# Kernel optimization log

Measured on AMD Instinct MI355X. Metric: run time of the kernel, lower is better.

Reference implementation:

```python
import jax, jax.numpy as jnp
import numpy as np

B, NP, NC, E, C = 4, 512, 256, 128, 32
NBUCKET = 20


def soft_one_hot_linspace(x, start=0.0, end=15.0, number=NBUCKET):
    # e3nn soft_one_hot_linspace, basis='smooth_finite', cutoff=True
    values = jnp.linspace(start, end, number + 2)[1:-1]
    step = (end - start) / (number + 1)
    diff = (x[..., None] - values) / step

    def sus(y):  # exp(-1/y) for y>0 else 0 (smooth unit step)
        return jnp.where(y > 0.0, jnp.exp(-1.0 / jnp.where(y > 0.0, y, 1.0)), 0.0)

    return 1.14136 * jnp.exp(2.0) * sus(diff + 1.0) * sus(1.0 - diff)


def _init_linear(k, fan_in, fan_out):
    k1, k2 = jax.random.split(k)
    bound = 1.0 / np.sqrt(fan_in)
    W = jax.random.uniform(k1, (fan_in, fan_out), jnp.float32, -bound, bound)
    b = jax.random.uniform(k2, (fan_out,), jnp.float32, -bound, bound)
    return W, b


def setup_inputs() -> dict:
    key = jax.random.key(0)
    ks = jax.random.split(key, 12)
    inp = {}
    inp["z"] = jax.random.normal(ks[0], (B, NP, NC, E), jnp.float32)
    inp["z_mask"] = jax.random.randint(ks[1], (B, NP, NC), 0, 2) == 1
    inp["pocket_rep"] = jax.random.normal(ks[2], (B, NP, E), jnp.float32)
    inp["candidate_dis"] = jax.random.uniform(ks[3], (B, NP, NC), jnp.float32) * 16.0
    inp["W_lin"], inp["b_lin"] = _init_linear(ks[4], E, C)
    inp["W_dis"], inp["b_dis"] = _init_linear(ks[5], NBUCKET, C)
    inp["W_energy"], inp["b_energy"] = _init_linear(ks[6], C, 1)
    inp["W_gate"], inp["b_gate"] = _init_linear(ks[7], C, 1)
    inp["bias"] = jnp.ones((1,), jnp.float32)
    inp["W_energy_p"], inp["b_energy_p"] = _init_linear(ks[8], C, 1)
    inp["W_gate_p"], inp["b_gate_p"] = _init_linear(ks[9], C, 1)
    inp["bias_p"] = jnp.ones((1,), jnp.float32)
    inp["W_out"], inp["b_out"] = _init_linear(ks[10], E * C, E)
    return inp


def reference(z, z_mask, pocket_rep, candidate_dis,
              W_lin, b_lin, W_dis, b_dis,
              W_energy, b_energy, W_gate, b_gate, bias,
              W_energy_p, b_energy_p, W_gate_p, b_gate_p, bias_p,
              W_out, b_out):
    b, n_p, n_c, e = z.shape
    c = W_lin.shape[1]
    # linear + transpose(3,1): [B,Np,Nc,E] -> [B,C,Nc,Np]
    zc = jnp.transpose(z @ W_lin + b_lin, (0, 3, 2, 1))
    # softmax over last dim (Np)
    zc = jax.nn.softmax(zc, axis=-1)
    # distance-bucket bias: [B,Np,Nc,20] -> [B,Np,Nc,C] -> view [B,C,Nc,Np]
    edge_emb = soft_one_hot_linspace(candidate_dis)
    dis_bias = (edge_emb @ W_dis + b_dis).reshape(b, c, n_c, n_p)
    zc = zc + dis_bias
    # z_mask.repeat(C,1,1).view(B,C,Nc,Np) -- literal torch element order
    mask_rep = jnp.tile(z_mask, (c, 1, 1)).reshape(b, c, n_c, n_p)
    zc = jnp.where(mask_rep, jnp.asarray(1e-09, zc.dtype), zc)
    # gated energy heads on z.transpose(3,1): [B,Np,Nc,C]
    zt = jnp.transpose(zc, (0, 3, 2, 1))
    zm = z_mask.astype(zc.dtype)
    pair_energy = (jax.nn.sigmoid(zt @ W_gate + b_gate) * (zt @ W_energy + b_energy))[..., 0] * zm
    affinity_pred = jax.nn.leaky_relu(bias + pair_energy.sum(axis=(-1, -2)))
    pair_energy_p = (jax.nn.sigmoid(zt @ W_gate_p + b_gate_p) * (zt @ W_energy_p + b_energy_p))[..., 0] * zm
    prmsd_pred = jax.nn.leaky_relu(bias_p + pair_energy_p.sum(axis=(-1, -2)))
    # ligand rep: bmm([B,C*Nc,Np], [B,Np,E]) -> [B,Nc,C*E] -> Linear
    lig = jnp.einsum('bcln,bne->bcle', zc, pocket_rep)  # [B,C,Nc,E]
    lig = jnp.transpose(lig, (0, 2, 1, 3)).reshape(b, n_c, c * e)
    ligand_rep = lig @ W_out + b_out
    return (ligand_rep, affinity_pred, prmsd_pred)
```

## Files before the change

### kernel.cpp

```cpp
#include <hip/hip_runtime.h>
#include <stdint.h>


typedef float f32x4 __attribute__((ext_vector_type(4)));
typedef short s16x8 __attribute__((ext_vector_type(8)));

#define DEV static __device__ __forceinline__

DEV unsigned short f2bf(float f) {
  unsigned u = __builtin_bit_cast(unsigned, f);
  u += 0x7FFFu + ((u >> 16) & 1u);
  return (unsigned short)(u >> 16);
}
DEV float bf2f(unsigned short h) {
  unsigned u = ((unsigned)h) << 16;
  return __builtin_bit_cast(float, u);
}

__global__ void prep_k(const float* __restrict__ wlin,
                       const float* __restrict__ pocket,
                       const float* __restrict__ wout,
                       const int* __restrict__ zmask,
                       const float* __restrict__ cdis,
                       const float* __restrict__ bout,
                       unsigned short* __restrict__ wtlin,
                       unsigned short* __restrict__ pt,
                       unsigned short* __restrict__ wto,
                       unsigned long long* __restrict__ zmb,
                       float* __restrict__ cdisT,
                       float* __restrict__ outp,
                       float* __restrict__ accg) {
  for (int i = blockIdx.x * 256 + threadIdx.x; i < 1970184; i += gridDim.x * 256) {
    if (i < 524288) {
      int np = i & 511, nc = (i >> 9) & 255, b = i >> 17;
      unsigned long long bal = __ballot(zmask[b * 131072 + np * 256 + nc] != 0);
      if ((i & 63) == 0) zmb[i >> 6] = bal;
    } else if (i < 1048576) {
      int o = i - 524288;
      int e = o >> 12, k = o & 4095;
      wto[o] = f2bf(wout[k * 128 + e]);
    } else if (i < 1310720) {
      int o = i - 1048576;
      int np = o & 511, r = o >> 9;
      int e = r & 127, b = r >> 7;
      pt[o] = f2bf(pocket[(b * 512 + np) * 128 + e]);
    } else if (i < 1314816) {
      int o = i - 1310720;
      int k = o & 127, c = o >> 7;
      wtlin[o] = f2bf(wlin[k * 32 + c]);
    } else if (i < 1314824) {
      accg[i - 1314816] = 0.0f;
    } else if (i < 1839112) {
      int o = i - 1314824;
      int c = o & 31, np5 = (o >> 5) & 15, nc = (o >> 9) & 255, b = o >> 17;
      cdisT[o] = cdis[(b * 512 + 16 * c + (nc >> 4)) * 256 + 16 * (nc & 15) + np5];
    } else {
      int o = i - 1839112;
      outp[o] = bout[o & 127];
    }
  }
}

extern __shared__ char smem[];

__global__ __launch_bounds__(256, 4) void mega_k(
    const float* __restrict__ z, const int* __restrict__ zmask,
    const float* __restrict__ cdisT,
    const float* __restrict__ wdis, const float* __restrict__ bdis_g,
    const float* __restrict__ wE, const float* __restrict__ bE,
    const float* __restrict__ wG, const float* __restrict__ bG,
    const float* __restrict__ wEp, const float* __restrict__ bEp,
    const float* __restrict__ wGp, const float* __restrict__ bGp,
    const unsigned short* __restrict__ wtlin,
    const unsigned short* __restrict__ pt,
    const unsigned long long* __restrict__ zmb,
    unsigned short* __restrict__ lig, float* __restrict__ accg) {
  const int nc = blockIdx.x, b = blockIdx.y;
  const int t = threadIdx.x;
  const int w = t >> 6, ln = t & 63;
  const int m16 = ln & 15, q = ln >> 4;

  unsigned short* T = (unsigned short*)smem;

  __shared__ float s_wd[640];
  __shared__ float s_bd[32];
  __shared__ float s_we[32], s_wg[32], s_wep[32], s_wgp[32];
  __shared__ float s_red[160];
  __shared__ float s_gmax[32], s_gsum[32];
  __shared__ unsigned long long s_mb[4][8];
  __shared__ float s_r8[8];

  if (t < 32) {
    s_bd[t] = bdis_g[t];
    s_we[t] = wE[t]; s_wg[t] = wG[t];
    s_wep[t] = wEp[t]; s_wgp[t] = wGp[t];
  }
  for (int i = t; i < 640; i += 256) s_wd[i] = wdis[i];
  for (int i = t; i < 2048; i += 256) {
    int cm = i >> 9, nn = i & 511;
    unsigned long long bal = __ballot(zmask[cm * 131072 + nc * 512 + nn] != 0);
    if ((i & 63) == 0) s_mb[cm][nn >> 6] = bal;
  }

  f32x4 acc1[8][2];
#pragma unroll
  for (int i = 0; i < 8; ++i) {
    acc1[i][0] = f32x4{0.f, 0.f, 0.f, 0.f};
    acc1[i][1] = f32x4{0.f, 0.f, 0.f, 0.f};
  }
  const float* zb = z + (size_t)b * 16777216 + (size_t)nc * 128;
  for (int k0 = 0; k0 < 128; k0 += 32) {
    s16x8 bf0 = *(const s16x8*)(wtlin + m16 * 128 + k0 + q * 8);
    s16x8 bf1 = *(const s16x8*)(wtlin + (16 + m16) * 128 + k0 + q * 8);
#pragma unroll
    for (int bt = 0; bt < 4; ++bt) {
      f32x4 z0[2], z1[2];
#pragma unroll
      for (int i = 0; i < 2; ++i) {
        int np = (w * 8 + bt * 2 + i) * 16 + m16;
        const float* p = zb + (size_t)np * 32768 + k0 + q * 8;
        z0[i] = *(const f32x4*)p;
        z1[i] = *(const f32x4*)(p + 4);
      }
#pragma unroll
      for (int i = 0; i < 2; ++i) {
        s16x8 af;
        af[0] = (short)f2bf(z0[i][0]); af[1] = (short)f2bf(z0[i][1]);
        af[2] = (short)f2bf(z0[i][2]); af[3] = (short)f2bf(z0[i][3]);
        af[4] = (short)f2bf(z1[i][0]); af[5] = (short)f2bf(z1[i][1]);
        af[6] = (short)f2bf(z1[i][2]); af[7] = (short)f2bf(z1[i][3]);
        int ai = bt * 2 + i;
        acc1[ai][0] = __builtin_amdgcn_mfma_f32_16x16x32_bf16(af, bf0, acc1[ai][0], 0, 0, 0);
        acc1[ai][1] = __builtin_amdgcn_mfma_f32_16x16x32_bf16(af, bf1, acc1[ai][1], 0, 0, 0);
      }
    }
  }

  float mx[2] = {-3.0e38f, -3.0e38f};
#pragma unroll
  for (int ai = 0; ai < 8; ++ai)
#pragma unroll
    for (int ct = 0; ct < 2; ++ct)
#pragma unroll
      for (int r = 0; r < 4; ++r) mx[ct] = fmaxf(mx[ct], acc1[ai][ct][r]);
#pragma unroll
  for (int ct = 0; ct < 2; ++ct) {
    float v = mx[ct];
    v = fmaxf(v, __shfl_xor(v, 16));
    v = fmaxf(v, __shfl_xor(v, 32));
    mx[ct] = v;
  }
  if (ln < 16) { s_red[ln * 5 + w] = mx[0]; s_red[(16 + ln) * 5 + w] = mx[1]; }
  __syncthreads();
  if (t < 32)
    s_gmax[t] = fmaxf(fmaxf(s_red[t * 5], s_red[t * 5 + 1]),
                      fmaxf(s_red[t * 5 + 2], s_red[t * 5 + 3]));
  __syncthreads();
  float sm[2] = {0.f, 0.f};
#pragma unroll
  for (int ct = 0; ct < 2; ++ct) {
    float g = s_gmax[ct * 16 + m16];
#pragma unroll
    for (int ai = 0; ai < 8; ++ai)
#pragma unroll
      for (int r = 0; r < 4; ++r) {
        float e = __expf(acc1[ai][ct][r] - g);
        acc1[ai][ct][r] = e;
        sm[ct] += e;
      }
  }
#pragma unroll
  for (int ct = 0; ct < 2; ++ct) {
    float v = sm[ct];
    v += __shfl_xor(v, 16);
    v += __shfl_xor(v, 32);
    sm[ct] = v;
  }
  if (ln < 16) { s_red[ln * 5 + w] = sm[0]; s_red[(16 + ln) * 5 + w] = sm[1]; }
  __syncthreads();
  if (t < 32)
    s_gsum[t] = 1.0f / (s_red[t * 5] + s_red[t * 5 + 1] + s_red[t * 5 + 2] + s_red[t * 5 + 3]);
  __syncthreads();

#pragma unroll
  for (int ct = 0; ct < 2; ++ct) {
    int c = ct * 16 + m16;
    float s = s_gsum[c];
#pragma unroll
    for (int ai = 0; ai < 8; ++ai) {
      int npb = (w * 8 + ai) * 16 + q * 4;
      unsigned lo = (unsigned)f2bf(acc1[ai][ct][0] * s) |
                    ((unsigned)f2bf(acc1[ai][ct][1] * s) << 16);
      unsigned hi = (unsigned)f2bf(acc1[ai][ct][2] * s) |
                    ((unsigned)f2bf(acc1[ai][ct][3] * s) << 16);
      *(uint2*)(T + c * 520 + npb) = make_uint2(lo, hi);
    }
  }
  __syncthreads();

  {
    const float SUSK = 8.4335794f;
    const float* cdb = cdisT + (size_t)(b * 256 + nc) * 512;
#pragma unroll
    for (int tt = 0; tt < 2; ++tt) {
      int task = t + tt * 256;
      int c = task & 31, np5 = task >> 5;
      float d = cdb[task];
      float val[32];
#pragma unroll
      for (int kk = 0; kk < 32; ++kk) val[kk] = s_bd[kk];
      for (int j = 0; j < 20; ++j) {
        float diff = d * (21.0f / 15.0f) - (float)(j + 1);
        float y1 = diff + 1.f, y2 = 1.f - diff;
        float u = 0.f;
        if (y1 > 0.f && y2 > 0.f) u = SUSK * __expf(-1.f / y1 - 1.f / y2);
#pragma unroll
        for (int kk = 0; kk < 32; ++kk) val[kk] += u * s_wd[j * 32 + kk];
      }
      int npb = np5 * 32;
      unsigned long long mw = s_mb[c & 3][npb >> 6];
#pragma unroll
      for (int kb2 = 0; kb2 < 4; ++kb2) {
        unsigned short* tp = T + c * 520 + npb + kb2 * 8;
        s16x8 tv = *(s16x8*)tp;
        s16x8 ov;
#pragma unroll
        for (int kk = 0; kk < 8; ++kk) {
          float x = bf2f((unsigned short)tv[kk]) + val[kb2 * 8 + kk];
          int mk = (int)((mw >> ((npb + kb2 * 8 + kk) & 63)) & 1ull);
          ov[kk] = (short)f2bf(mk ? 1e-9f : x);
        }
        *(s16x8*)tp = ov;
      }
    }
  }
  __syncthreads();

  {
    float aff = 0.f, prm = 0.f;
    const float bg0 = bG[0], be0 = bE[0], bgp0 = bGp[0], bep0 = bEp[0];
    const unsigned long long* zw = zmb + (size_t)(b * 256 + nc) * 8;
#pragma unroll
    for (int s = 0; s < 2; ++s) {
      int np = s * 256 + t;
      float g = bg0, e = be0, gp = bgp0, ep = bep0;
      for (int c = 0; c < 32; ++c) {
        float tv = bf2f(T[c * 520 + np]);
        g += tv * s_wg[c]; e += tv * s_we[c];
        gp += tv * s_wgp[c]; ep += tv * s_wep[c];
      }
      if ((zw[np >> 6] >> (np & 63)) & 1ull) {
        aff += e / (1.f + __expf(-g));
        prm += ep / (1.f + __expf(-gp));
      }
    }
#pragma unroll
    for (int d = 32; d >= 1; d >>= 1) {
      aff += __shfl_xor(aff, d);
      prm += __shfl_xor(prm, d);
    }
    if (ln == 0) { s_r8[w] = aff; s_r8[4 + w] = prm; }
    __syncthreads();
    if (t == 0) {
      atomicAdd(accg + b, s_r8[0] + s_r8[1] + s_r8[2] + s_r8[3]);
      atomicAdd(accg + 4 + b, s_r8[4] + s_r8[5] + s_r8[6] + s_r8[7]);
    }
  }

  {
    f32x4 a5[2][2];
    a5[0][0] = f32x4{0.f, 0.f, 0.f, 0.f}; a5[0][1] = a5[0][0];
    a5[1][0] = a5[0][0]; a5[1][1] = a5[0][0];
    const unsigned short* ptb = pt + b * 65536;
    for (int k0 = 0; k0 < 512; k0 += 32) {
      s16x8 aT0 = *(const s16x8*)(T + m16 * 520 + k0 + q * 8);
      s16x8 aT1 = *(const s16x8*)(T + (16 + m16) * 520 + k0 + q * 8);
      s16x8 bP0 = *(const s16x8*)(ptb + (w * 32 + m16) * 512 + k0 + q * 8);
      s16x8 bP1 = *(const s16x8*)(ptb + (w * 32 + 16 + m16) * 512 + k0 + q * 8);
      a5[0][0] = __builtin_amdgcn_mfma_f32_16x16x32_bf16(aT0, bP0, a5[0][0], 0, 0, 0);
      a5[0][1] = __builtin_amdgcn_mfma_f32_16x16x32_bf16(aT0, bP1, a5[0][1], 0, 0, 0);
      a5[1][0] = __builtin_amdgcn_mfma_f32_16x16x32_bf16(aT1, bP0, a5[1][0], 0, 0, 0);
      a5[1][1] = __builtin_amdgcn_mfma_f32_16x16x32_bf16(aT1, bP1, a5[1][1], 0, 0, 0);
    }
    unsigned short* lg = lig + (size_t)(b * 256 + nc) * 4096;
#pragma unroll
    for (int mt = 0; mt < 2; ++mt)
#pragma unroll
      for (int u = 0; u < 2; ++u)
#pragma unroll
        for (int r = 0; r < 4; ++r) {
          int c = mt * 16 + q * 4 + r;
          int e = w * 32 + u * 16 + m16;
          lg[c * 128 + e] = f2bf(a5[mt][u][r]);
        }
  }
}

__global__ __launch_bounds__(256, 2) void proj_k(
    const unsigned short* __restrict__ lig, const unsigned short* __restrict__ wto,
    const float* __restrict__ accg, const float* __restrict__ bias,
    const float* __restrict__ biasp, float* __restrict__ outp) {
  const int mb = blockIdx.x, ks = blockIdx.y;
  const int t = threadIdx.x, w = t >> 6, ln = t & 63;
  const int m16 = ln & 15, q = ln >> 4;
  f32x4 acc[2][8];
#pragma unroll
  for (int mt = 0; mt < 2; ++mt)
#pragma unroll
    for (int nt = 0; nt < 8; ++nt) acc[mt][nt] = f32x4{0.f, 0.f, 0.f, 0.f};
  const int kb = ks * 256;
  for (int k0 = 0; k0 < 256; k0 += 32) {
    s16x8 af[2], bf[8];
#pragma unroll
    for (int mt = 0; mt < 2; ++mt)
      af[mt] = *(const s16x8*)(lig + (size_t)(mb * 128 + (w * 2 + mt) * 16 + m16) * 4096 + kb + k0 + q * 8);
#pragma unroll
    for (int nt = 0; nt < 8; ++nt)
      bf[nt] = *(const s16x8*)(wto + (size_t)(nt * 16 + m16) * 4096 + kb + k0 + q * 8);
#pragma unroll
    for (int mt = 0; mt < 2; ++mt)
#pragma unroll
      for (int nt = 0; nt < 8; ++nt)
        acc[mt][nt] = __builtin_amdgcn_mfma_f32_16x16x32_bf16(af[mt], bf[nt], acc[mt][nt], 0, 0, 0);
  }
#pragma unroll
  for (int mt = 0; mt < 2; ++mt)
#pragma unroll
    for (int nt = 0; nt < 8; ++nt)
#pragma unroll
      for (int r = 0; r < 4; ++r)
        atomicAdd(outp + (size_t)(mb * 128 + (w * 2 + mt) * 16 + q * 4 + r) * 128 + nt * 16 + m16,
                  acc[mt][nt][r]);
  if (mb == 0 && ks == 0 && t < 8) {
    float base = (t < 4) ? bias[0] : biasp[0];
    float x = base + accg[t];
    outp[131072 + t] = (x >= 0.f) ? x : 0.01f * x;
  }
}

extern "C" void kernel_launch(void* const* d_in, const int* in_sizes, int n_in,
                              void* d_out, int out_size, void* d_ws, size_t ws_size,
                              hipStream_t stream) {
  const float* z      = (const float*)d_in[0];
  const int*   zmask  = (const int*)d_in[1];
  const float* pocket = (const float*)d_in[2];
  const float* cdis   = (const float*)d_in[3];
  const float* wlin   = (const float*)d_in[4];
  const float* wdis   = (const float*)d_in[6];
  const float* bdis   = (const float*)d_in[7];
  const float* wE     = (const float*)d_in[8];
  const float* bE     = (const float*)d_in[9];
  const float* wG     = (const float*)d_in[10];
  const float* bG     = (const float*)d_in[11];
  const float* bias   = (const float*)d_in[12];
  const float* wEp    = (const float*)d_in[13];
  const float* bEp    = (const float*)d_in[14];
  const float* wGp    = (const float*)d_in[15];
  const float* bGp    = (const float*)d_in[16];
  const float* biasp  = (const float*)d_in[17];
  const float* wout   = (const float*)d_in[18];
  const float* bout   = (const float*)d_in[19];

  char* ws = (char*)d_ws;
  float* accg                  = (float*)(ws + 0);
  unsigned short* wtlin        = (unsigned short*)(ws + 1024);
  unsigned long long* zmb      = (unsigned long long*)(ws + 16384);
  unsigned short* pt           = (unsigned short*)(ws + 131072);
  float* cdisT                 = (float*)(ws + 655360);
  unsigned short* wto          = (unsigned short*)(ws + 2752512);
  unsigned short* lig          = (unsigned short*)(ws + 4194304);
  float* outp = (float*)d_out;

  prep_k<<<1024, 256, 0, stream>>>(wlin, pocket, wout, zmask, cdis, bout,
                                   wtlin, pt, wto, zmb, cdisT, outp, accg);
  mega_k<<<dim3(256, 4), 256, 33280, stream>>>(z, zmask, cdisT, wdis, bdis,
      wE, bE, wG, bG, wEp, bEp, wGp, bGp, wtlin, pt, zmb, lig, accg);
  proj_k<<<dim3(8, 16), 256, 0, stream>>>(lig, wto, accg, bias, biasp, outp);
}
```

Baseline: 471.7 us.

## Replace split-K atomic projection with full-K tiles and fused bias

The output projection kernel no longer splits K across 16 blocks and accumulates with atomics. Each of 32 blocks now computes a 32x128 output tile over the full K=4096 and writes the result with b_out added directly, so the prep kernel no longer pre-fills the output with the bias. The float-to-bf16 conversion also switches to the HIP intrinsic. The cost is far less parallelism in the projection (32 blocks of 4 waves, each running a long serial K loop), which could make that stage slower even though atomics and the bias pass are gone.

```diff
diff --git a/kernel.cpp b/kernel.cpp
--- a/kernel.cpp
+++ b/kernel.cpp
@@ -1,4 +1,5 @@
 #include <hip/hip_runtime.h>
+#include <hip/hip_bf16.h>
 #include <stdint.h>
 
 
@@ -8,9 +9,7 @@
 #define DEV static __device__ __forceinline__
 
 DEV unsigned short f2bf(float f) {
-  unsigned u = __builtin_bit_cast(unsigned, f);
-  u += 0x7FFFu + ((u >> 16) & 1u);
-  return (unsigned short)(u >> 16);
+  return __builtin_bit_cast(unsigned short, __float2bfloat16(f));
 }
 DEV float bf2f(unsigned short h) {
   unsigned u = ((unsigned)h) << 16;
@@ -22,15 +21,13 @@
                        const float* __restrict__ wout,
                        const int* __restrict__ zmask,
                        const float* __restrict__ cdis,
-                       const float* __restrict__ bout,
                        unsigned short* __restrict__ wtlin,
                        unsigned short* __restrict__ pt,
                        unsigned short* __restrict__ wto,
                        unsigned long long* __restrict__ zmb,
                        float* __restrict__ cdisT,
-                       float* __restrict__ outp,
                        float* __restrict__ accg) {
-  for (int i = blockIdx.x * 256 + threadIdx.x; i < 1970184; i += gridDim.x * 256) {
+  for (int i = blockIdx.x * 256 + threadIdx.x; i < 1839112; i += gridDim.x * 256) {
     if (i < 524288) {
       int np = i & 511, nc = (i >> 9) & 255, b = i >> 17;
       unsigned long long bal = __ballot(zmask[b * 131072 + np * 256 + nc] != 0);
@@ -50,13 +47,10 @@
       wtlin[o] = f2bf(wlin[k * 32 + c]);
     } else if (i < 1314824) {
       accg[i - 1314816] = 0.0f;
-    } else if (i < 1839112) {
+    } else {
       int o = i - 1314824;
       int c = o & 31, np5 = (o >> 5) & 15, nc = (o >> 9) & 255, b = o >> 17;
       cdisT[o] = cdis[(b * 512 + 16 * c + (nc >> 4)) * 256 + 16 * (nc & 15) + np5];
-    } else {
-      int o = i - 1839112;
-      outp[o] = bout[o & 127];
     }
   }
 }
@@ -125,10 +119,10 @@
 #pragma unroll
       for (int i = 0; i < 2; ++i) {
         s16x8 af;
-        af[0] = (short)f2bf(z0[i][0]); af[1] = (short)f2bf(z0[i][1]);
-        af[2] = (short)f2bf(z0[i][2]); af[3] = (short)f2bf(z0[i][3]);
-        af[4] = (short)f2bf(z1[i][0]); af[5] = (short)f2bf(z1[i][1]);
-        af[6] = (short)f2bf(z1[i][2]); af[7] = (short)f2bf(z1[i][3]);
+#pragma unroll
+        for (int j = 0; j < 4; ++j) af[j] = (short)f2bf(z0[i][j]);
+#pragma unroll
+        for (int j = 0; j < 4; ++j) af[4 + j] = (short)f2bf(z1[i][j]);
         int ai = bt * 2 + i;
         acc1[ai][0] = __builtin_amdgcn_mfma_f32_16x16x32_bf16(af, bf0, acc1[ai][0], 0, 0, 0);
         acc1[ai][1] = __builtin_amdgcn_mfma_f32_16x16x32_bf16(af, bf1, acc1[ai][1], 0, 0, 0);
@@ -296,42 +290,41 @@
   }
 }
 
-__global__ __launch_bounds__(256, 2) void proj_k(
+__global__ __launch_bounds__(256, 4) void proj_k(
     const unsigned short* __restrict__ lig, const unsigned short* __restrict__ wto,
     const float* __restrict__ accg, const float* __restrict__ bias,
-    const float* __restrict__ biasp, float* __restrict__ outp) {
-  const int mb = blockIdx.x, ks = blockIdx.y;
+    const float* __restrict__ biasp, const float* __restrict__ bout,
+    float* __restrict__ outp) {
+  const int mb = blockIdx.x;
   const int t = threadIdx.x, w = t >> 6, ln = t & 63;
   const int m16 = ln & 15, q = ln >> 4;
-  f32x4 acc[2][8];
+  f32x4 acc[2][2];
+  acc[0][0] = f32x4{0.f, 0.f, 0.f, 0.f}; acc[0][1] = acc[0][0];
+  acc[1][0] = acc[0][0]; acc[1][1] = acc[0][0];
+  for (int k0 = 0; k0 < 4096; k0 += 32) {
+    s16x8 af[2], bf[2];
+#pragma unroll
+    for (int mt = 0; mt < 2; ++mt)
+      af[mt] = *(const s16x8*)(lig + (size_t)(mb * 32 + mt * 16 + m16) * 4096 + k0 + q * 8);
+#pragma unroll
+    for (int u = 0; u < 2; ++u)
+      bf[u] = *(const s16x8*)(wto + (size_t)(w * 32 + u * 16 + m16) * 4096 + k0 + q * 8);
+#pragma unroll
+    for (int mt = 0; mt < 2; ++mt)
+#pragma unroll
+      for (int u = 0; u < 2; ++u)
+        acc[mt][u] = __builtin_amdgcn_mfma_f32_16x16x32_bf16(af[mt], bf[u], acc[mt][u], 0, 0, 0);
+  }
+  float bo[2] = {bout[w * 32 + m16], bout[w * 32 + 16 + m16]};
 #pragma unroll
   for (int mt = 0; mt < 2; ++mt)
 #pragma unroll
-    for (int nt = 0; nt < 8; ++nt) acc[mt][nt] = f32x4{0.f, 0.f, 0.f, 0.f};
-  const int kb = ks * 256;
-  for (int k0 = 0; k0 < 256; k0 += 32) {
-    s16x8 af[2], bf[8];
-#pragma unroll
-    for (int mt = 0; mt < 2; ++mt)
-      af[mt] = *(const s16x8*)(lig + (size_t)(mb * 128 + (w * 2 + mt) * 16 + m16) * 4096 + kb + k0 + q * 8);
-#pragma unroll
-    for (int nt = 0; nt < 8; ++nt)
-      bf[nt] = *(const s16x8*)(wto + (size_t)(nt * 16 + m16) * 4096 + kb + k0 + q * 8);
-#pragma unroll
-    for (int mt = 0; mt < 2; ++mt)
-#pragma unroll
-      for (int nt = 0; nt < 8; ++nt)
-        acc[mt][nt] = __builtin_amdgcn_mfma_f32_16x16x32_bf16(af[mt], bf[nt], acc[mt][nt], 0, 0, 0);
-  }
-#pragma unroll
-  for (int mt = 0; mt < 2; ++mt)
-#pragma unroll
-    for (int nt = 0; nt < 8; ++nt)
+    for (int u = 0; u < 2; ++u)
 #pragma unroll
       for (int r = 0; r < 4; ++r)
-        atomicAdd(outp + (size_t)(mb * 128 + (w * 2 + mt) * 16 + q * 4 + r) * 128 + nt * 16 + m16,
-                  acc[mt][nt][r]);
-  if (mb == 0 && ks == 0 && t < 8) {
+        outp[(size_t)(mb * 32 + mt * 16 + q * 4 + r) * 128 + w * 32 + u * 16 + m16] =
+            acc[mt][u][r] + bo[u];
+  if (mb == 0 && t < 8) {
     float base = (t < 4) ? bias[0] : biasp[0];
     float x = base + accg[t];
     outp[131072 + t] = (x >= 0.f) ? x : 0.01f * x;
@@ -371,9 +364,9 @@
   unsigned short* lig          = (unsigned short*)(ws + 4194304);
   float* outp = (float*)d_out;
 
-  prep_k<<<1024, 256, 0, stream>>>(wlin, pocket, wout, zmask, cdis, bout,
-                                   wtlin, pt, wto, zmb, cdisT, outp, accg);
+  prep_k<<<1024, 256, 0, stream>>>(wlin, pocket, wout, zmask, cdis,
+                                   wtlin, pt, wto, zmb, cdisT, accg);
   mega_k<<<dim3(256, 4), 256, 33280, stream>>>(z, zmask, cdisT, wdis, bdis,
       wE, bE, wG, bG, wEp, bEp, wGp, bGp, wtlin, pt, zmb, lig, accg);
-  proj_k<<<dim3(8, 16), 256, 0, stream>>>(lig, wto, accg, bias, biasp, outp);
-}
+  proj_k<<<32, 256, 0, stream>>>(lig, wto, accg, bias, biasp, bout, outp);
+}
```

New measurement: 527.6 us. 1.12x slower.
